# Performance work log

Hardware: AMD Instinct MI355X
Metric: run time of the kernel (lower is better)

The kernel has to match this reference:

```python
import jax, jax.numpy as jnp
import numpy as np

LN_EPS = 1e-5

def _gelu(x):
    # matches the module's custom gelu: x * sigmoid(1.702 * x)
    return x * jax.nn.sigmoid(1.702 * x)

def setup_inputs() -> dict:
    key = jax.random.key(0)
    k1, k2, k3, k4 = jax.random.split(key, 4)
    B, d_in, d_out, E = 4096, 768, 1024, 10
    x = jax.random.normal(k1, (B, d_in), dtype=jnp.float32)
    x_cls_logits = jax.random.normal(k2, (B, E), dtype=jnp.float32)
    # expert weights (torch Linear stored transposed; here [in, out] acting as x @ W)
    W1 = jax.random.normal(k3, (E, d_in, d_out), dtype=jnp.float32) * (d_in ** -0.5)
    W2 = jax.random.normal(k4, (E, d_out, d_out), dtype=jnp.float32) * (d_out ** -0.5)
    ln_gamma = jnp.ones((E, d_out), dtype=jnp.float32)
    ln_beta = jnp.zeros((E, d_out), dtype=jnp.float32)
    return {"x": x, "x_cls_logits": x_cls_logits, "W1": W1, "W2": W2,
            "ln_gamma": ln_gamma, "ln_beta": ln_beta}

def reference(x, x_cls_logits, W1, W2, ln_gamma, ln_beta):
    B = x.shape[0]
    # top-1 routing: each sample goes to expert argmax(x_cls)
    cls = jnp.argmax(x_cls_logits, axis=1)                       # [B] int
    # compute all experts densely, then select per sample (grouped equivalent of
    # the per-sample Python-loop dispatch in the original forward)
    embed1_all = jnp.einsum('bi,eio->beo', x, W1)                # [B,E,d_out]
    embed2_all = jnp.einsum('beo,eop->bep', _gelu(embed1_all), W2)  # [B,E,d_out]
    s_all = embed1_all + embed2_all                              # [B,E,d_out]
    rows = jnp.arange(B)
    s = s_all[rows, cls]                                         # [B,d_out]
    # per-expert LayerNorm params gathered per sample
    g = ln_gamma[cls]                                            # [B,d_out]
    b = ln_beta[cls]                                             # [B,d_out]
    mean = jnp.mean(s, axis=-1, keepdims=True)
    var = jnp.mean(jnp.square(s - mean), axis=-1, keepdims=True)
    y = (s - mean) * jax.lax.rsqrt(var + LN_EPS) * g + b
    # L2 normalize embeddings
    out = y / jnp.linalg.norm(y, axis=-1, keepdims=True)
    return out, x_cls_logits
```

## Files before the change

kernel.cpp:

```cpp
#include <hip/hip_runtime.h>
#include <math.h>

#define BSAMP 4096
#define D_IN  768
#define D_OUT 1024
#define NEXP  10
#define LN_EPS 1e-5f
#define STEPS1 (D_IN / 64)
#define STEPS2 (D_OUT / 64)

typedef __attribute__((ext_vector_type(8))) short bf16x8;
typedef __attribute__((ext_vector_type(4))) float f32x4;

__device__ __forceinline__ float b2f(unsigned short u) {
    union { unsigned int i; float f; } v; v.i = ((unsigned int)u) << 16; return v.f;
}
__device__ __forceinline__ unsigned short f2b(float f) {
    union { float f; unsigned int i; } v; v.f = f;
    unsigned int x = v.i;
    unsigned int r = (x + 0x7fffu + ((x >> 16) & 1u)) >> 16;
    return (unsigned short)r;
}


__global__ void k4_init(int* counts, int* cursor) {
    int t = threadIdx.x;
    if (t < 16) { counts[t] = 0; cursor[t] = 0; }
}

__global__ void k4_router(const float* __restrict__ logits,
                          int* __restrict__ cls, int* __restrict__ counts,
                          float* __restrict__ out1) {
    int b = blockIdx.x * 256 + threadIdx.x;
    if (b >= BSAMP) return;
    const float* L = logits + (size_t)b * NEXP;
    float best = L[0]; int be = 0;
    #pragma unroll
    for (int e = 0; e < NEXP; e++) {
        float v = L[e];
        out1[(size_t)b * NEXP + e] = v;
        if (v > best) { best = v; be = e; }
    }
    cls[b] = be;
    atomicAdd(&counts[be], 1);
}

__global__ void k4_scan(const int* counts, int* offs, int* cursor) {
    if (threadIdx.x == 0) {
        int s = 0;
        for (int e = 0; e < NEXP; e++) { offs[e] = s; cursor[e] = s; s += counts[e]; }
        offs[NEXP] = s;
    }
}

__global__ void k4_scatter(const int* __restrict__ cls, int* __restrict__ cursor,
                           int* __restrict__ idx) {
    int b = blockIdx.x * 256 + threadIdx.x;
    if (b >= BSAMP) return;
    int p = atomicAdd(&cursor[cls[b]], 1);
    idx[p] = b;
}

__global__ __launch_bounds__(256)
void k5_xcvt(const float* __restrict__ X, unsigned short* __restrict__ xb) {
    int i = (blockIdx.x * 256 + threadIdx.x) * 8;
    float4 v0 = *(const float4*)(X + i);
    float4 v1 = *(const float4*)(X + i + 4);
    unsigned short t[8] = { f2b(v0.x), f2b(v0.y), f2b(v0.z), f2b(v0.w),
                            f2b(v1.x), f2b(v1.y), f2b(v1.z), f2b(v1.w) };
    *(bf16x8*)(xb + i) = *(bf16x8*)t;
}

__global__ __launch_bounds__(256)
void k4_cvt(const float* __restrict__ W, unsigned short* __restrict__ Wt, int K) {
    const int t  = threadIdx.x;
    const int kt = blockIdx.x;
    const int e  = blockIdx.z;
    const int n  = blockIdx.y * 256 + t;
    const int KT = K >> 5;
    const float* src = W + ((size_t)e * K + (size_t)kt * 32) * D_OUT + n;
    unsigned short v[32];
    #pragma unroll
    for (int j = 0; j < 32; j++) v[j] = f2b(src[(size_t)j * D_OUT]);
    const int nt = n >> 7, nn = n & 127;
    unsigned short* dst = Wt + ((((size_t)e * 8 + nt) * KT + kt) << 12) + nn * 32;
    #pragma unroll
    for (int j = 0; j < 4; j++)
        *(bf16x8*)&dst[j * 8] = *(bf16x8*)&v[j * 8];
}


#define GLDS(srcp, dstp) __builtin_amdgcn_global_load_lds( \
    (const __attribute__((address_space(1))) unsigned int*)(srcp), \
    (__attribute__((address_space(3))) unsigned int*)(dstp), 16, 0, 0)

#define STAGE_A(Ab, t) do { \
    _Pragma("unroll") \
    for (int j = 0; j < 2; j++) { \
        int c = tid + j * 256; \
        GLDS(aRow + (t) * 64 + (c >> 6) * 8, (Ab) + c * 8); \
    } \
} while (0)

#define STAGE_B(Bb, t) do { \
    _Pragma("unroll") \
    for (int j = 0; j < 4; j++) { \
        int c = tid + j * 256; \
        int kc = c >> 7; \
        GLDS(bPanel + ((size_t)(2 * (t) + (kc >> 2)) << 12) + (c & 127) * 32 + (kc & 3) * 8, \
             (Bb) + c * 8); \
    } \
} while (0)

#define COMPUTE(Ab, Bb) do { \
    _Pragma("unroll") \
    for (int s = 0; s < 2; s++) { \
        const unsigned short* ab_ = (Ab) + (s * 4 + quad) * 512; \
        const unsigned short* bb_ = (Bb) + (s * 4 + quad) * 1024; \
        bf16x8 a0 = *(const bf16x8*)&ab_[(wrow + l16) * 8]; \
        bf16x8 a1 = *(const bf16x8*)&ab_[(wrow + 16 + l16) * 8]; \
        bf16x8 b0 = *(const bf16x8*)&bb_[(wcol + l16) * 8]; \
        bf16x8 b1 = *(const bf16x8*)&bb_[(wcol + 16 + l16) * 8]; \
        bf16x8 b2 = *(const bf16x8*)&bb_[(wcol + 32 + l16) * 8]; \
        bf16x8 b3 = *(const bf16x8*)&bb_[(wcol + 48 + l16) * 8]; \
        acc[0][0] = __builtin_amdgcn_mfma_f32_16x16x32_bf16(a0, b0, acc[0][0], 0, 0, 0); \
        acc[0][1] = __builtin_amdgcn_mfma_f32_16x16x32_bf16(a0, b1, acc[0][1], 0, 0, 0); \
        acc[0][2] = __builtin_amdgcn_mfma_f32_16x16x32_bf16(a0, b2, acc[0][2], 0, 0, 0); \
        acc[0][3] = __builtin_amdgcn_mfma_f32_16x16x32_bf16(a0, b3, acc[0][3], 0, 0, 0); \
        acc[1][0] = __builtin_amdgcn_mfma_f32_16x16x32_bf16(a1, b0, acc[1][0], 0, 0, 0); \
        acc[1][1] = __builtin_amdgcn_mfma_f32_16x16x32_bf16(a1, b1, acc[1][1], 0, 0, 0); \
        acc[1][2] = __builtin_amdgcn_mfma_f32_16x16x32_bf16(a1, b2, acc[1][2], 0, 0, 0); \
        acc[1][3] = __builtin_amdgcn_mfma_f32_16x16x32_bf16(a1, b3, acc[1][3], 0, 0, 0); \
    } \
} while (0)

__global__ __launch_bounds__(256)
void k6_gemm1(const unsigned short* __restrict__ xb, const unsigned short* __restrict__ W1t,
              const int* __restrict__ offs, const int* __restrict__ idx,
              unsigned short* __restrict__ e1g, unsigned short* __restrict__ g1g) {
    const int e = blockIdx.z;
    const int rowStart = offs[e] + blockIdx.y * 64;
    const int rowEnd = offs[e + 1];
    if (rowStart >= rowEnd) return;
    const int nt = blockIdx.x;

    __shared__ __align__(16) unsigned short A0[64 * 64], A1[64 * 64];
    __shared__ __align__(16) unsigned short B0[128 * 64], B1[128 * 64];
    __shared__ int rowIdxL[64];

    const int tid  = threadIdx.x;
    const int lane = tid & 63;
    const int wave = tid >> 6;
    const int quad = lane >> 4;
    const int l16  = lane & 15;
    const int wrow = (wave & 1) * 32;
    const int wcol = (wave >> 1) * 64;

    if (tid < 64) {
        int p = rowStart + tid;
        rowIdxL[tid] = idx[p < rowEnd ? p : rowEnd - 1];
    }
    __syncthreads();

    const unsigned short* aRow   = xb + (size_t)rowIdxL[tid & 63] * D_IN;
    const unsigned short* bPanel = W1t + ((((size_t)e * 8 + nt) * (D_IN / 32)) << 12);

    f32x4 acc[2][4];
    const f32x4 zf = {0.f, 0.f, 0.f, 0.f};
    #pragma unroll
    for (int r = 0; r < 2; r++)
        #pragma unroll
        for (int c = 0; c < 4; c++) acc[r][c] = zf;

    STAGE_A(A0, 0); STAGE_B(B0, 0);
    __syncthreads();
    for (int t = 0; t < STEPS1; t += 2) {
        STAGE_A(A1, t + 1); STAGE_B(B1, t + 1);
        COMPUTE(A0, B0);
        __syncthreads();
        if (t + 2 < STEPS1) { STAGE_A(A0, t + 2); STAGE_B(B0, t + 2); }
        COMPUTE(A1, B1);
        __syncthreads();
    }

    const int n0 = nt * 128;
    #pragma unroll
    for (int r = 0; r < 2; r++)
        #pragma unroll
        for (int q = 0; q < 4; q++) {
            int m = wrow + r * 16 + quad * 4 + q;
            int pp = rowStart + m;
            if (pp < rowEnd) {
                unsigned short* ep = e1g + (size_t)pp * D_OUT + n0 + wcol + l16;
                unsigned short* gp = g1g + (size_t)pp * D_OUT + n0 + wcol + l16;
                #pragma unroll
                for (int c = 0; c < 4; c++) {
                    unsigned short vb = f2b(acc[r][c][q]);
                    ep[c * 16] = vb;
                    float v = b2f(vb);
                    gp[c * 16] = f2b(v / (1.0f + __expf(-1.702f * v)));
                }
            }
        }
}

__global__ __launch_bounds__(256)
void k6_gemm2(const unsigned short* __restrict__ g1g, const unsigned short* __restrict__ e1g,
              const unsigned short* __restrict__ W2t,
              const int* __restrict__ offs, const int* __restrict__ idx,
              float* __restrict__ out0) {
    const int e = blockIdx.z;
    const int rowStart = offs[e] + blockIdx.y * 64;
    const int rowEnd = offs[e + 1];
    if (rowStart >= rowEnd) return;
    const int nt = blockIdx.x;

    __shared__ __align__(16) unsigned short A0[64 * 64], A1[64 * 64];
    __shared__ __align__(16) unsigned short B0[128 * 64], B1[128 * 64];
    __shared__ int rowIdxL[64];

    const int tid  = threadIdx.x;
    const int lane = tid & 63;
    const int wave = tid >> 6;
    const int quad = lane >> 4;
    const int l16  = lane & 15;
    const int wrow = (wave & 1) * 32;
    const int wcol = (wave >> 1) * 64;

    if (tid < 64) {
        int p = rowStart + tid;
        int ps = p < rowEnd ? p : rowEnd - 1;
        rowIdxL[tid] = idx[ps];
    }
    __syncthreads();

    int ap = rowStart + (tid & 63);
    const unsigned short* aRow   = g1g + (size_t)(ap < rowEnd ? ap : rowEnd - 1) * D_OUT;
    const unsigned short* bPanel = W2t + ((((size_t)e * 8 + nt) * (D_OUT / 32)) << 12);

    f32x4 acc[2][4];
    const f32x4 zf = {0.f, 0.f, 0.f, 0.f};
    #pragma unroll
    for (int r = 0; r < 2; r++)
        #pragma unroll
        for (int c = 0; c < 4; c++) acc[r][c] = zf;

    STAGE_A(A0, 0); STAGE_B(B0, 0);
    __syncthreads();
    for (int t = 0; t < STEPS2; t += 2) {
        STAGE_A(A1, t + 1); STAGE_B(B1, t + 1);
        COMPUTE(A0, B0);
        __syncthreads();
        if (t + 2 < STEPS2) { STAGE_A(A0, t + 2); STAGE_B(B0, t + 2); }
        COMPUTE(A1, B1);
        __syncthreads();
    }

    const int n0 = nt * 128;
    #pragma unroll
    for (int r = 0; r < 2; r++)
        #pragma unroll
        for (int q = 0; q < 4; q++) {
            int m = wrow + r * 16 + quad * 4 + q;
            int pp = rowStart + m;
            if (pp < rowEnd) {
                const unsigned short* ep = e1g + (size_t)pp * D_OUT + n0 + wcol + l16;
                float* op = out0 + (size_t)rowIdxL[m] * D_OUT + n0 + wcol + l16;
                #pragma unroll
                for (int c = 0; c < 4; c++)
                    op[c * 16] = acc[r][c][q] + b2f(ep[c * 16]);
            }
        }
}

__global__ __launch_bounds__(256)
void k4_ln(float* __restrict__ out0, const int* __restrict__ cls,
           const float* __restrict__ gam, const float* __restrict__ bet) {
    const int wave = threadIdx.x >> 6;
    const int lane = threadIdx.x & 63;
    const int b = blockIdx.x * 4 + wave;
    const int e = cls[b];

    float* row = out0 + (size_t)b * D_OUT + lane * 16;
    float v[16];
    #pragma unroll
    for (int j = 0; j < 4; j++) {
        float4 t = *(const float4*)(row + j * 4);
        v[j*4] = t.x; v[j*4+1] = t.y; v[j*4+2] = t.z; v[j*4+3] = t.w;
    }

    float sum = 0.f, sq = 0.f;
    #pragma unroll
    for (int j = 0; j < 16; j++) { sum += v[j]; sq += v[j] * v[j]; }
    #pragma unroll
    for (int o = 32; o; o >>= 1) { sum += __shfl_xor(sum, o, 64); sq += __shfl_xor(sq, o, 64); }
    float mean = sum * (1.0f / 1024.0f);
    float var = sq * (1.0f / 1024.0f) - mean * mean;
    float inv = rsqrtf(var + LN_EPS);

    const float* gp = gam + (size_t)e * D_OUT + lane * 16;
    const float* bp = bet + (size_t)e * D_OUT + lane * 16;
    float y[16]; float y2 = 0.f;
    #pragma unroll
    for (int j = 0; j < 16; j++) {
        y[j] = (v[j] - mean) * inv * gp[j] + bp[j];
        y2 += y[j] * y[j];
    }
    #pragma unroll
    for (int o = 32; o; o >>= 1) y2 += __shfl_xor(y2, o, 64);
    float rn = rsqrtf(y2);

    #pragma unroll
    for (int j = 0; j < 4; j++) {
        float4 t = { y[j*4] * rn, y[j*4+1] * rn, y[j*4+2] * rn, y[j*4+3] * rn };
        *(float4*)(row + j * 4) = t;
    }
}

extern "C" void kernel_launch(void* const* d_in, const int* in_sizes, int n_in,
                              void* d_out, int out_size, void* d_ws, size_t ws_size,
                              hipStream_t stream) {
    const float* x   = (const float*)d_in[0];
    const float* lg  = (const float*)d_in[1];
    const float* W1  = (const float*)d_in[2];
    const float* W2  = (const float*)d_in[3];
    const float* gam = (const float*)d_in[4];
    const float* bet = (const float*)d_in[5];
    float* out0 = (float*)d_out;
    float* out1 = out0 + (size_t)BSAMP * D_OUT;

    char* ws = (char*)d_ws;
    int* counts = (int*)ws;
    int* offs   = counts + 16;
    int* cursor = offs + 16;
    int* cls    = cursor + 16;
    int* idx    = cls + BSAMP;
    unsigned short* Wt  = (unsigned short*)(ws + 65536);
    unsigned short* e1g = (unsigned short*)(ws + 65536 + 22020096);
    unsigned short* g1g = e1g + (size_t)BSAMP * D_OUT;
    unsigned short* xb  = g1g + (size_t)BSAMP * D_OUT;

    k4_init<<<1, 64, 0, stream>>>(counts, cursor);
    k4_router<<<16, 256, 0, stream>>>(lg, cls, counts, out1);
    k4_scan<<<1, 64, 0, stream>>>(counts, offs, cursor);
    k4_scatter<<<16, 256, 0, stream>>>(cls, cursor, idx);

    k5_xcvt<<<BSAMP * D_IN / (256 * 8), 256, 0, stream>>>(x, xb);

    dim3 gc1(D_IN / 32, 4, NEXP);
    k4_cvt<<<gc1, 256, 0, stream>>>(W1, Wt, D_IN);
    dim3 g1(8, 64, NEXP);
    k6_gemm1<<<g1, 256, 0, stream>>>(xb, Wt, offs, idx, e1g, g1g);

    dim3 gc2(D_OUT / 32, 4, NEXP);
    k4_cvt<<<gc2, 256, 0, stream>>>(W2, Wt, D_OUT);
    dim3 g2(8, 64, NEXP);
    k6_gemm2<<<g2, 256, 0, stream>>>(g1g, e1g, Wt, offs, idx, out0);

    k4_ln<<<BSAMP / 4, 256, 0, stream>>>(out0, cls, gam, bet);
}
```

Measured before the change: 244.4 us.

## Fuse routing, scan, scatter and all weight/input conversions into one prep kernel

Replaces seven small launches (init, router, scan, scatter, x conversion, and two weight conversions) with a single kernel. Block 0 does routing, counting, scan and scatter using shared-memory atomics, and the remaining blocks convert W1, W2 and x to bf16. W2 now gets its own workspace buffer, so its conversion no longer has to wait for gemm1. This removes launch gaps and serial dependencies. The cost is that block 0 runs the whole routing step serially over 4096 samples, which can become a long tail.

```diff
diff --git a/kernel.cpp b/kernel.cpp
--- a/kernel.cpp
+++ b/kernel.cpp
@@ -9,6 +9,11 @@
 #define STEPS1 (D_IN / 64)
 #define STEPS2 (D_OUT / 64)
 
+#define NB_CVT1 (D_IN / 32 * 4 * NEXP)
+#define NB_CVT2 (D_OUT / 32 * 4 * NEXP)
+#define NB_XCVT (BSAMP * D_IN / 2048)
+#define NB_PREP (1 + NB_CVT1 + NB_CVT2 + NB_XCVT)
+
 typedef __attribute__((ext_vector_type(8))) short bf16x8;
 typedef __attribute__((ext_vector_type(4))) float f32x4;
 
@@ -23,61 +28,14 @@
 }
 
 
-__global__ void k4_init(int* counts, int* cursor) {
-    int t = threadIdx.x;
-    if (t < 16) { counts[t] = 0; cursor[t] = 0; }
-}
-
-__global__ void k4_router(const float* __restrict__ logits,
-                          int* __restrict__ cls, int* __restrict__ counts,
-                          float* __restrict__ out1) {
-    int b = blockIdx.x * 256 + threadIdx.x;
-    if (b >= BSAMP) return;
-    const float* L = logits + (size_t)b * NEXP;
-    float best = L[0]; int be = 0;
-    #pragma unroll
-    for (int e = 0; e < NEXP; e++) {
-        float v = L[e];
-        out1[(size_t)b * NEXP + e] = v;
-        if (v > best) { best = v; be = e; }
-    }
-    cls[b] = be;
-    atomicAdd(&counts[be], 1);
-}
-
-__global__ void k4_scan(const int* counts, int* offs, int* cursor) {
-    if (threadIdx.x == 0) {
-        int s = 0;
-        for (int e = 0; e < NEXP; e++) { offs[e] = s; cursor[e] = s; s += counts[e]; }
-        offs[NEXP] = s;
-    }
-}
-
-__global__ void k4_scatter(const int* __restrict__ cls, int* __restrict__ cursor,
-                           int* __restrict__ idx) {
-    int b = blockIdx.x * 256 + threadIdx.x;
-    if (b >= BSAMP) return;
-    int p = atomicAdd(&cursor[cls[b]], 1);
-    idx[p] = b;
-}
-
-__global__ __launch_bounds__(256)
-void k5_xcvt(const float* __restrict__ X, unsigned short* __restrict__ xb) {
-    int i = (blockIdx.x * 256 + threadIdx.x) * 8;
-    float4 v0 = *(const float4*)(X + i);
-    float4 v1 = *(const float4*)(X + i + 4);
-    unsigned short t[8] = { f2b(v0.x), f2b(v0.y), f2b(v0.z), f2b(v0.w),
-                            f2b(v1.x), f2b(v1.y), f2b(v1.z), f2b(v1.w) };
-    *(bf16x8*)(xb + i) = *(bf16x8*)t;
-}
-
-__global__ __launch_bounds__(256)
-void k4_cvt(const float* __restrict__ W, unsigned short* __restrict__ Wt, int K) {
-    const int t  = threadIdx.x;
-    const int kt = blockIdx.x;
-    const int e  = blockIdx.z;
-    const int n  = blockIdx.y * 256 + t;
+__device__ __forceinline__ void cvt_body(const float* __restrict__ W,
+                                         unsigned short* __restrict__ Wt,
+                                         int K, int i, int tid) {
     const int KT = K >> 5;
+    const int kt = i % KT;
+    const int rest = i / KT;
+    const int n = (rest & 3) * 256 + tid;
+    const int e = rest >> 2;
     const float* src = W + ((size_t)e * K + (size_t)kt * 32) * D_OUT + n;
     unsigned short v[32];
     #pragma unroll
@@ -87,6 +45,71 @@
     #pragma unroll
     for (int j = 0; j < 4; j++)
         *(bf16x8*)&dst[j * 8] = *(bf16x8*)&v[j * 8];
+}
+
+__global__ __launch_bounds__(256)
+void k7_prep(const float* __restrict__ logits, const float* __restrict__ X,
+             const float* __restrict__ W1, const float* __restrict__ W2,
+             float* __restrict__ out1, int* __restrict__ cls,
+             int* __restrict__ idx, int* __restrict__ offs,
+             unsigned short* __restrict__ xb, unsigned short* __restrict__ W1t,
+             unsigned short* __restrict__ W2t) {
+    const int tid = threadIdx.x;
+    const int blk = blockIdx.x;
+
+    if (blk == 0) {
+        __shared__ int cnt[NEXP];
+        __shared__ int cur[NEXP];
+        __shared__ int offsL[NEXP + 1];
+        if (tid < NEXP) cnt[tid] = 0;
+        __syncthreads();
+
+        int be[16];
+        #pragma unroll
+        for (int j = 0; j < 16; j++) {
+            int b = tid + 256 * j;
+            const float* L = logits + (size_t)b * NEXP;
+            float best = L[0]; int e0 = 0;
+            #pragma unroll
+            for (int e = 0; e < NEXP; e++) {
+                float v = L[e];
+                out1[(size_t)b * NEXP + e] = v;
+                if (v > best) { best = v; e0 = e; }
+            }
+            be[j] = e0;
+            cls[b] = e0;
+            atomicAdd(&cnt[e0], 1);
+        }
+        __syncthreads();
+        if (tid == 0) {
+            int s = 0;
+            for (int e = 0; e < NEXP; e++) { offsL[e] = s; cur[e] = s; s += cnt[e]; }
+            offsL[NEXP] = s;
+        }
+        __syncthreads();
+        if (tid <= NEXP) offs[tid] = offsL[tid];
+        #pragma unroll
+        for (int j = 0; j < 16; j++) {
+            int b = tid + 256 * j;
+            int p = atomicAdd(&cur[be[j]], 1);
+            idx[p] = b;
+        }
+        return;
+    }
+
+    int i = blk - 1;
+    if (i < NB_CVT1) { cvt_body(W1, W1t, D_IN, i, tid); return; }
+    i -= NB_CVT1;
+    if (i < NB_CVT2) { cvt_body(W2, W2t, D_OUT, i, tid); return; }
+    i -= NB_CVT2;
+    {
+        int o = (i * 256 + tid) * 8;
+        float4 v0 = *(const float4*)(X + o);
+        float4 v1 = *(const float4*)(X + o + 4);
+        unsigned short t[8] = { f2b(v0.x), f2b(v0.y), f2b(v0.z), f2b(v0.w),
+                                f2b(v1.x), f2b(v1.y), f2b(v1.z), f2b(v1.w) };
+        *(bf16x8*)(xb + o) = *(bf16x8*)t;
+    }
 }
 
 
@@ -330,32 +353,23 @@
     float* out1 = out0 + (size_t)BSAMP * D_OUT;
 
     char* ws = (char*)d_ws;
-    int* counts = (int*)ws;
-    int* offs   = counts + 16;
-    int* cursor = offs + 16;
-    int* cls    = cursor + 16;
-    int* idx    = cls + BSAMP;
-    unsigned short* Wt  = (unsigned short*)(ws + 65536);
-    unsigned short* e1g = (unsigned short*)(ws + 65536 + 22020096);
+    int* offs = (int*)ws;
+    int* cls  = offs + 16;
+    int* idx  = cls + BSAMP;
+    unsigned short* W1t = (unsigned short*)(ws + 65536);
+    unsigned short* W2t = W1t + (size_t)NEXP * D_IN * D_OUT;
+    unsigned short* e1g = W2t + (size_t)NEXP * D_OUT * D_OUT;
     unsigned short* g1g = e1g + (size_t)BSAMP * D_OUT;
     unsigned short* xb  = g1g + (size_t)BSAMP * D_OUT;
 
-    k4_init<<<1, 64, 0, stream>>>(counts, cursor);
-    k4_router<<<16, 256, 0, stream>>>(lg, cls, counts, out1);
-    k4_scan<<<1, 64, 0, stream>>>(counts, offs, cursor);
-    k4_scatter<<<16, 256, 0, stream>>>(cls, cursor, idx);
-
-    k5_xcvt<<<BSAMP * D_IN / (256 * 8), 256, 0, stream>>>(x, xb);
-
-    dim3 gc1(D_IN / 32, 4, NEXP);
-    k4_cvt<<<gc1, 256, 0, stream>>>(W1, Wt, D_IN);
+    k7_prep<<<NB_PREP, 256, 0, stream>>>(lg, x, W1, W2, out1, cls, idx, offs,
+                                         xb, W1t, W2t);
+
     dim3 g1(8, 64, NEXP);
-    k6_gemm1<<<g1, 256, 0, stream>>>(xb, Wt, offs, idx, e1g, g1g);
-
-    dim3 gc2(D_OUT / 32, 4, NEXP);
-    k4_cvt<<<gc2, 256, 0, stream>>>(W2, Wt, D_OUT);
+    k6_gemm1<<<g1, 256, 0, stream>>>(xb, W1t, offs, idx, e1g, g1g);
+
     dim3 g2(8, 64, NEXP);
-    k6_gemm2<<<g2, 256, 0, stream>>>(g1g, e1g, Wt, offs, idx, out0);
+    k6_gemm2<<<g2, 256, 0, stream>>>(g1g, e1g, W2t, offs, idx, out0);
 
     k4_ln<<<BSAMP / 4, 256, 0, stream>>>(out0, cls, gam, bet);
 }
```

New measurement: 209.8 us. -14.1%, faster.
